# Optimization experiments

Measured on AMD Instinct MI355X. Metric: run time of the kernel, lower is better.

Reference implementation:

```python
import jax, jax.numpy as jnp
import numpy as np

NUM_HEADS = 12


def get_rel_pos(q_size, k_size, rel_pos):
    # rel_pos: (2*max(q,k)-1, C). Here q_size==k_size so no interpolation needed.
    q_coords = jnp.arange(q_size)[:, None] * max(k_size / q_size, 1.0)
    k_coords = jnp.arange(k_size)[None, :] * max(q_size / k_size, 1.0)
    rel = (q_coords - k_coords) + (k_size - 1) * max(q_size / k_size, 1.0)
    return rel_pos[rel.astype(jnp.int32)]  # (q_size, k_size, C)


def add_decomposed_rel_pos(attn, q, rel_pos_h, rel_pos_w, q_size, k_size):
    q_h, q_w = q_size
    k_h, k_w = k_size
    Rh = get_rel_pos(q_h, k_h, rel_pos_h)  # (q_h,k_h,C)
    Rw = get_rel_pos(q_w, k_w, rel_pos_w)  # (q_w,k_w,C)
    B, _, C = q.shape  # B = num_heads * batch
    r_q = q.reshape(B, q_h, q_w, C)
    rel_h = jnp.einsum('bhwc,hkc->bhwk', r_q, Rh)  # (B,q_h,q_w,k_h)
    rel_w = jnp.einsum('bhwc,wkc->bhwk', r_q, Rw)  # (B,q_h,q_w,k_w)
    attn = attn.reshape(B, q_h, q_w, k_h, k_w)
    attn = attn + rel_h[:, :, :, :, None] + rel_w[:, :, :, None, :]
    return attn.reshape(B, q_h * q_w, k_h * k_w)


def setup_inputs() -> dict:
    key = jax.random.key(0)
    ks = jax.random.split(key, 7)
    B, H, W, dim = 128, 14, 14, 768
    head_dim = dim // NUM_HEADS
    return {
        'x': jax.random.normal(ks[0], (B, H, W, dim), dtype=jnp.float32),
        'qkv_w': jax.random.normal(ks[1], (dim, 3 * dim), dtype=jnp.float32) * 0.02,
        'qkv_b': jax.random.normal(ks[2], (3 * dim,), dtype=jnp.float32) * 0.02,
        'proj_w': jax.random.normal(ks[3], (dim, dim), dtype=jnp.float32) * 0.02,
        'proj_b': jax.random.normal(ks[4], (dim,), dtype=jnp.float32) * 0.02,
        'rel_pos_h': jax.random.normal(ks[5], (2 * H - 1, head_dim), dtype=jnp.float32) * 0.02,
        'rel_pos_w': jax.random.normal(ks[6], (2 * W - 1, head_dim), dtype=jnp.float32) * 0.02,
    }


def reference(x, qkv_w, qkv_b, proj_w, proj_b, rel_pos_h, rel_pos_w):
    B, H, W, dim = x.shape
    nh = NUM_HEADS
    hd = dim // nh
    scale = hd ** -0.5
    L = H * W
    # qkv projection: (B,H,W,3*dim) -> (3, nh*B, L, hd)
    qkv = x.reshape(B, L, dim) @ qkv_w + qkv_b
    qkv = qkv.reshape(B, L, 3, nh, hd)
    qkv = jnp.transpose(qkv, (2, 3, 0, 1, 4)).reshape(3, nh * B, L, hd)
    q, k, v = qkv[0], qkv[1], qkv[2]
    attn = jnp.einsum('bqc,bkc->bqk', q * scale, k)  # (nh*B, L, L)
    attn = add_decomposed_rel_pos(attn, q, rel_pos_h, rel_pos_w, (H, W), (H, W))
    attn = jax.nn.softmax(attn, axis=-1)
    out = jnp.einsum('bqk,bkc->bqc', attn, v)  # (nh*B, L, hd)
    out = out.reshape(nh, B, H, W, hd)
    out = jnp.transpose(out, (1, 2, 3, 0, 4)).reshape(B, H, W, dim)
    return out @ proj_w + proj_b
```

## Files before the change

kernel.cpp:

```cpp
#include <hip/hip_runtime.h>
#include <stdint.h>

typedef unsigned short u16;
typedef __bf16 bf16x8 __attribute__((ext_vector_type(8)));
typedef u16 u16x8 __attribute__((ext_vector_type(8)));
typedef float f32x4 __attribute__((ext_vector_type(4)));

#define MFMA16(a,b,c) __builtin_amdgcn_mfma_f32_16x16x32_bf16((a),(b),(c),0,0,0)
#define GLOAD16(gp, lp) __builtin_amdgcn_global_load_lds( \
    (const __attribute__((address_space(1))) void*)(gp), \
    (__attribute__((address_space(3))) void*)(lp), 16, 0, 0)

__device__ __forceinline__ u16 f2bf(float f) {
  union { float f; uint32_t u; } v; v.f = f;
  return (u16)((v.u + 0x7FFFu + ((v.u >> 16) & 1u)) >> 16);
}
__device__ __forceinline__ float bits2f(uint32_t u) {
  union { uint32_t u; float f; } v; v.u = u; return v.f;
}
__device__ __forceinline__ uint32_t cvtpk(float lo, float hi) {
  uint32_t r;
  asm("v_cvt_pk_bf16_f32 %0, %1, %2" : "=v"(r) : "v"(lo), "v"(hi));
  return r;
}
__device__ __forceinline__ int4 pack8(const u16* v) {
  int4 r;
  r.x = (int)((uint32_t)v[0] | ((uint32_t)v[1] << 16));
  r.y = (int)((uint32_t)v[2] | ((uint32_t)v[3] << 16));
  r.z = (int)((uint32_t)v[4] | ((uint32_t)v[5] << 16));
  r.w = (int)((uint32_t)v[6] | ((uint32_t)v[7] << 16));
  return r;
}

__global__ void k_cvt(const float* __restrict__ in, u16* __restrict__ out, int n4) {
  int i = blockIdx.x * 256 + threadIdx.x;
  int stride = gridDim.x * 256;
  for (; i < n4; i += stride) {
    float4 v = reinterpret_cast<const float4*>(in)[i];
    ushort4 o;
    o.x = f2bf(v.x); o.y = f2bf(v.y); o.z = f2bf(v.z); o.w = f2bf(v.w);
    reinterpret_cast<ushort4*>(out)[i] = o;
  }
}

__global__ void k_transpose(const float* __restrict__ in, u16* __restrict__ out, int R, int C) {
  __shared__ float t[32][33];
  int tx = threadIdx.x & 31, ty = threadIdx.x >> 5;
  int c0 = blockIdx.x * 32, r0 = blockIdx.y * 32;
  #pragma unroll
  for (int i = 0; i < 4; i++)
    t[ty + i*8][tx] = in[(size_t)(r0 + ty + i*8) * C + (c0 + tx)];
  __syncthreads();
  #pragma unroll
  for (int i = 0; i < 4; i++)
    out[(size_t)(c0 + ty + i*8) * R + (r0 + tx)] = f2bf(t[tx][ty + i*8]);
}

__global__ __launch_bounds__(512, 2) void k_qkv256(
    const u16* __restrict__ A, const u16* __restrict__ BT, const float* __restrict__ bias,
    u16* __restrict__ qo, u16* __restrict__ ko, u16* __restrict__ vo)
{
  __shared__ u16 SMEM[65536];

  int bid0 = blockIdx.x;
  int xcd = bid0 & 7, idx = bid0 >> 3;
  int base = (xcd < 2) ? xcd * 111 : 2 * 111 + (xcd - 2) * 110;
  int wgid = base + idx;
  int mt = wgid / 9, nt = wgid - (wgid / 9) * 9;

  int tid = threadIdx.x, lane = tid & 63, w = tid >> 6;
  int g = lane >> 4, c4 = lane & 15;
  int wr = w >> 2, wc = w & 3;

  int srow = lane >> 2;
  int pslot = (lane & 3) ^ ((lane >> 3) & 3);
  int cidA = w * 2;

  const u16* pA1 = A + (size_t)(mt * 256 + cidA * 16 + srow) * 768 + pslot * 8;
  const u16* pA2 = pA1 + 16 * 768;
  const u16* pB1 = BT + (size_t)(nt * 256 + cidA * 16 + srow) * 768 + pslot * 8;
  const u16* pB2 = pB1 + 16 * 768;

  int rsel = g ^ ((c4 >> 1) & 3);
  int aoff = wr * 4096 + c4 * 32 + rsel * 8;
  int boff = wc * 2048 + c4 * 32 + rsel * 8;

  f32x4 acc[8][4];
  f32x4 z4 = {0.f, 0.f, 0.f, 0.f};
  #pragma unroll
  for (int f = 0; f < 8; f++)
    #pragma unroll
    for (int fc = 0; fc < 4; fc++) acc[f][fc] = z4;

  #pragma unroll
  for (int kk = 0; kk < 3; kk++) {
    u16* dA = SMEM + kk * 8192;
    GLOAD16(pA1 + kk * 32, dA + cidA * 512);
    GLOAD16(pA2 + kk * 32, dA + (cidA + 1) * 512);
    u16* dB = SMEM + 32768 + kk * 8192;
    GLOAD16(pB1 + kk * 32, dB + cidA * 512);
    GLOAD16(pB2 + kk * 32, dB + (cidA + 1) * 512);
  }
  asm volatile("s_waitcnt vmcnt(8)" ::: "memory");
  __builtin_amdgcn_s_barrier();

  for (int k = 0; k < 24; ++k) {
    const u16* As = SMEM + (k & 3) * 8192;
    const u16* Bs = SMEM + 32768 + (k & 3) * 8192;
    bf16x8 bfr[4], afr[4];
    #pragma unroll
    for (int fc = 0; fc < 4; fc++) bfr[fc] = *(const bf16x8*)(Bs + boff + fc * 512);
    #pragma unroll
    for (int f = 0; f < 4; f++) afr[f] = *(const bf16x8*)(As + aoff + f * 512);
    if (k < 21) {
      u16* d = SMEM + ((k + 3) & 3) * 8192;
      GLOAD16(pA1 + (k + 3) * 32, d + cidA * 512);
      GLOAD16(pA2 + (k + 3) * 32, d + (cidA + 1) * 512);
      asm volatile("s_waitcnt vmcnt(6)" ::: "memory");
    } else if (k == 21) {
      asm volatile("s_waitcnt vmcnt(0)" ::: "memory");
    }
    __builtin_amdgcn_s_barrier();
    __builtin_amdgcn_s_setprio(1);
    #pragma unroll
    for (int f = 0; f < 4; f++)
      #pragma unroll
      for (int fc = 0; fc < 4; fc++)
        acc[f][fc] = MFMA16(afr[f], bfr[fc], acc[f][fc]);
    __builtin_amdgcn_s_setprio(0);

    #pragma unroll
    for (int f = 0; f < 4; f++) afr[f] = *(const bf16x8*)(As + aoff + (4 + f) * 512);
    if (k < 21) {
      u16* d = SMEM + 32768 + ((k + 3) & 3) * 8192;
      GLOAD16(pB1 + (k + 3) * 32, d + cidA * 512);
      GLOAD16(pB2 + (k + 3) * 32, d + (cidA + 1) * 512);
      asm volatile("s_waitcnt vmcnt(6)" ::: "memory");
    }
    __builtin_amdgcn_s_barrier();
    __builtin_amdgcn_s_setprio(1);
    #pragma unroll
    for (int f = 0; f < 4; f++)
      #pragma unroll
      for (int fc = 0; fc < 4; fc++)
        acc[4 + f][fc] = MFMA16(afr[f], bfr[fc], acc[4 + f][fc]);
    __builtin_amdgcn_s_setprio(0);
  }

  int i3 = nt / 3;
  u16* dst = (i3 == 0) ? qo : (i3 == 1) ? ko : vo;
  int head = (nt - i3 * 3) * 4 + wc;
  float bsv[4];
  #pragma unroll
  for (int fc = 0; fc < 4; fc++) bsv[fc] = bias[nt * 256 + wc * 64 + fc * 16 + c4];

  int mbase = mt * 256 + wr * 128 + g * 4;
  #pragma unroll
  for (int f = 0; f < 8; f++) {
    #pragma unroll
    for (int j = 0; j < 4; j++) {
      int mm = mbase + f * 16 + j;
      int bb2 = mm / 196, ll = mm - bb2 * 196;
      size_t ro = (size_t)((head * 128 + bb2) * 196 + ll) * 64;
      #pragma unroll
      for (int fc = 0; fc < 4; fc++)
        dst[ro + fc * 16 + c4] = f2bf(acc[f][fc][j] + bsv[fc]);
    }
  }
}

__global__ __launch_bounds__(256, 2) void k_proj256(
    const u16* __restrict__ A, const u16* __restrict__ BT, const float* __restrict__ bias,
    float* __restrict__ out)
{
  __shared__ u16 SMEM[32768];

  int bid0 = blockIdx.x;
  int bid = (bid0 & 7) * 147 + (bid0 >> 3);
  int nt = bid % 6, mt = bid / 6;

  int tid = threadIdx.x, lane = tid & 63, w = tid >> 6;
  int g = lane >> 4, c4 = lane & 15;
  int wr = w >> 1, wc = w & 1;

  int srow = lane >> 2;
  int pslot = (lane & 3) ^ ((lane >> 3) & 3);
  int cidA = w * 2;

  const u16* pA1 = A + (size_t)(mt * 128 + cidA * 16 + srow) * 768 + pslot * 8;
  const u16* pA2 = pA1 + 16 * 768;
  const u16* pB1 = BT + (size_t)(nt * 128 + cidA * 16 + srow) * 768 + pslot * 8;
  const u16* pB2 = pB1 + 16 * 768;

  int rsel = g ^ ((c4 >> 1) & 3);
  int aoff = wr * 2048 + c4 * 32 + rsel * 8;
  int boff = wc * 2048 + c4 * 32 + rsel * 8;

  f32x4 acc[4][4];
  f32x4 z4 = {0.f, 0.f, 0.f, 0.f};
  #pragma unroll
  for (int f = 0; f < 4; f++)
    #pragma unroll
    for (int fc = 0; fc < 4; fc++) acc[f][fc] = z4;

  #pragma unroll
  for (int kk = 0; kk < 3; kk++) {
    u16* dA = SMEM + kk * 4096;
    GLOAD16(pA1 + kk * 32, dA + cidA * 512);
    GLOAD16(pA2 + kk * 32, dA + (cidA + 1) * 512);
    u16* dB = SMEM + 16384 + kk * 4096;
    GLOAD16(pB1 + kk * 32, dB + cidA * 512);
    GLOAD16(pB2 + kk * 32, dB + (cidA + 1) * 512);
  }
  asm volatile("s_waitcnt vmcnt(8)" ::: "memory");
  __builtin_amdgcn_s_barrier();

  for (int k = 0; k < 24; ++k) {
    const u16* As = SMEM + (k & 3) * 4096;
    const u16* Bs = SMEM + 16384 + (k & 3) * 4096;
    bf16x8 bfr[4], afr[4];
    #pragma unroll
    for (int fc = 0; fc < 4; fc++) bfr[fc] = *(const bf16x8*)(Bs + boff + fc * 512);
    #pragma unroll
    for (int f = 0; f < 4; f++) afr[f] = *(const bf16x8*)(As + aoff + f * 512);
    if (k < 21) {
      u16* dA = SMEM + ((k + 3) & 3) * 4096;
      GLOAD16(pA1 + (k + 3) * 32, dA + cidA * 512);
      GLOAD16(pA2 + (k + 3) * 32, dA + (cidA + 1) * 512);
      u16* dB = SMEM + 16384 + ((k + 3) & 3) * 4096;
      GLOAD16(pB1 + (k + 3) * 32, dB + cidA * 512);
      GLOAD16(pB2 + (k + 3) * 32, dB + (cidA + 1) * 512);
      asm volatile("s_waitcnt vmcnt(8)" ::: "memory");
    } else if (k == 21) {
      asm volatile("s_waitcnt vmcnt(4)" ::: "memory");
    } else if (k == 22) {
      asm volatile("s_waitcnt vmcnt(0)" ::: "memory");
    }
    __builtin_amdgcn_s_barrier();
    __builtin_amdgcn_s_setprio(1);
    #pragma unroll
    for (int f = 0; f < 4; f++)
      #pragma unroll
      for (int fc = 0; fc < 4; fc++)
        acc[f][fc] = MFMA16(afr[f], bfr[fc], acc[f][fc]);
    __builtin_amdgcn_s_setprio(0);
    __builtin_amdgcn_s_barrier();
  }

  #pragma unroll
  for (int fc = 0; fc < 4; fc++) {
    int n0 = nt * 128 + wc * 64 + fc * 16 + c4;
    float bs = bias[n0];
    #pragma unroll
    for (int fr = 0; fr < 4; fr++)
      #pragma unroll
      for (int j = 0; j < 4; j++) {
        int m = mt * 128 + wr * 64 + fr * 16 + g * 4 + j;
        out[(size_t)m * 768 + n0] = acc[fr][fc][j] + bs;
      }
  }
}

#define VP 232
__global__ __launch_bounds__(256, 2) void k_attn(
    const u16* __restrict__ Q, const u16* __restrict__ Kg, const u16* __restrict__ Vg,
    const u16* __restrict__ RPH, const u16* __restrict__ RPW, u16* __restrict__ Ows)
{
  __shared__ u16 K64[208 * 64];
  __shared__ u16 Krel[208 * 40];
  __shared__ u16 VT[64 * VP];
  __shared__ u16 Qrel[4][16 * 40];

  int bh = blockIdx.x;
  int hh = bh >> 7, bb = bh & 127;
  int tid = threadIdx.x, lane = tid & 63, w = tid >> 6;
  int g = lane >> 4, c4 = lane & 15;

  const u16* kbase = Kg + (size_t)bh * 12544;
  const u16* vbase = Vg + (size_t)bh * 12544;
  const u16* qbase = Q + (size_t)bh * 12544;

  for (int ch = tid; ch < 1664; ch += 256) {
    int row = ch >> 3, s = ch & 7;
    u16 outv[8];
    if (row < 196) {
      u16x8 v = *(const u16x8*)(kbase + row * 64 + s * 8);
      #pragma unroll
      for (int e = 0; e < 8; e++)
        outv[e] = f2bf(bits2f((uint32_t)v[e] << 16) * 0.125f);
    } else {
      #pragma unroll
      for (int e = 0; e < 8; e++) outv[e] = 0;
    }
    *(int4*)(K64 + row * 64 + ((s ^ (row & 7)) * 8)) = pack8(outv);
  }
  if (tid < 208) {
    int k = tid;
    int kh = k / 14, kw2 = k - kh * 14;
    #pragma unroll
    for (int s = 0; s < 5; s++) {
      u16 vals[8];
      #pragma unroll
      for (int e = 0; e < 8; e++) {
        int c = s * 8 + e;
        u16 x = 0;
        if (k < 196) {
          if (c == kh) x = 0x3F80;
          else if (c == 14 + kw2) x = 0x3F80;
        } else {
          if (c == 28) x = 0x3F80;
        }
        vals[e] = x;
      }
      *(int4*)(Krel + k * 40 + s * 8) = pack8(vals);
    }
  }
  for (int i = tid; i < 2048; i += 256) {
    int chn = i >> 5, c = 192 + (i & 31);
    if (c >= 196 && c < VP) VT[chn * VP + c] = 0;
  }
  for (int ch2 = tid; ch2 < 784; ch2 += 256) {
    int kp = ch2 >> 3, cb = ch2 & 7;
    int key = kp * 2, cz = cb * 8;
    u16x8 a = *(const u16x8*)(vbase + key * 64 + cz);
    u16x8 b2 = *(const u16x8*)(vbase + (key + 1) * 64 + cz);
    int kk = key & 31;
    int colp = (key >> 5) * 32 + ((kk & 15) >> 2) * 8 + (kk & 3) + ((kk >> 4) << 2);
    #pragma unroll
    for (int j = 0; j < 8; j++) {
      uint32_t pk = (uint32_t)a[j] | ((uint32_t)b2[j] << 16);
      *(uint32_t*)(VT + (cz + j) * VP + colp) = pk;
    }
  }
  __syncthreads();

  int t1 = 16 + c4; if (t1 > 26) t1 = 26;
  bf16x8 rh00 = *(const bf16x8*)(RPH + c4 * 64 + g * 8);
  bf16x8 rh01 = *(const bf16x8*)(RPH + c4 * 64 + 32 + g * 8);
  bf16x8 rh10 = *(const bf16x8*)(RPH + t1 * 64 + g * 8);
  bf16x8 rh11 = *(const bf16x8*)(RPH + t1 * 64 + 32 + g * 8);
  bf16x8 rw00 = *(const bf16x8*)(RPW + c4 * 64 + g * 8);
  bf16x8 rw01 = *(const bf16x8*)(RPW + c4 * 64 + 32 + g * 8);
  bf16x8 rw10 = *(const bf16x8*)(RPW + t1 * 64 + g * 8);
  bf16x8 rw11 = *(const bf16x8*)(RPW + t1 * 64 + 32 + g * 8);

  f32x4 z4 = {0.f, 0.f, 0.f, 0.f};

  for (int qt = w; qt < 13; qt += 4) {
    int qi = qt * 16 + c4;
    int qrow = qi > 195 ? 195 : qi;
    bf16x8 qa0 = *(const bf16x8*)(qbase + qrow * 64 + g * 8);
    bf16x8 qa1 = *(const bf16x8*)(qbase + qrow * 64 + 32 + g * 8);

    u16* Qr = (u16*)Qrel[w];
    {
      int4 zz = {0, 0, 0, 0};
      *(int4*)(Qr + lane * 8) = zz;
      if (lane < 16) *(int4*)(Qr + 512 + lane * 8) = zz;
      if (g == 0) Qr[c4 * 40 + 28] = f2bf(-30000.f);
    }

    int qh = qi / 14;
    int qwv = qi - qh * 14;

    f32x4 e0 = MFMA16(rh00, qa0, z4); e0 = MFMA16(rh01, qa1, e0);
    f32x4 e1 = MFMA16(rh10, qa0, z4); e1 = MFMA16(rh11, qa1, e1);
    #pragma unroll
    for (int tt = 0; tt < 2; tt++) {
      f32x4 e = tt ? e1 : e0;
      #pragma unroll
      for (int j = 0; j < 4; j++) {
        int t = tt * 16 + 4 * g + j;
        int kh = qh + 13 - t;
        if ((unsigned)kh <= 13u) Qr[c4 * 40 + kh] = f2bf(e[j]);
      }
    }
    f32x4 f0 = MFMA16(rw00, qa0, z4); f0 = MFMA16(rw01, qa1, f0);
    f32x4 f1 = MFMA16(rw10, qa0, z4); f1 = MFMA16(rw11, qa1, f1);
    #pragma unroll
    for (int tt = 0; tt < 2; tt++) {
      f32x4 e = tt ? f1 : f0;
      #pragma unroll
      for (int j = 0; j < 4; j++) {
        int t = tt * 16 + 4 * g + j;
        int kw3 = qwv + 13 - t;
        if ((unsigned)kw3 <= 13u) Qr[c4 * 40 + 14 + kw3] = f2bf(e[j]);
      }
    }

    bf16x8 qrelB = *(const bf16x8*)(Qr + c4 * 40 + g * 8);

    f32x4 St[13];
    #pragma unroll
    for (int i = 0; i < 13; i++) {
      int key = i * 16 + c4;
      const u16* kr = K64 + key * 64;
      int sw = key & 7;
      bf16x8 kb0 = *(const bf16x8*)(kr + ((g ^ sw) * 8));
      bf16x8 kb1 = *(const bf16x8*)(kr + (((4 + g) ^ sw) * 8));
      f32x4 acc = MFMA16(kb0, qa0, z4);
      acc = MFMA16(kb1, qa1, acc);
      bf16x8 krl = *(const bf16x8*)(Krel + key * 40 + g * 8);
      St[i] = MFMA16(krl, qrelB, acc);
    }

    float mx = -3.0e38f;
    #pragma unroll
    for (int i = 0; i < 13; i++)
      #pragma unroll
      for (int j = 0; j < 4; j++) mx = fmaxf(mx, St[i][j]);
    mx = fmaxf(mx, __shfl_xor(mx, 16));
    mx = fmaxf(mx, __shfl_xor(mx, 32));

    float ls = 0.f;
    f32x4 O[4] = {z4, z4, z4, z4};
    #pragma unroll
    for (int p = 0; p < 7; p++) {
      float pe[8];
      #pragma unroll
      for (int j2 = 0; j2 < 4; j2++) { pe[j2] = __expf(St[2 * p][j2] - mx); ls += pe[j2]; }
      if (p < 6) {
        #pragma unroll
        for (int j2 = 0; j2 < 4; j2++) { pe[4 + j2] = __expf(St[2 * p + 1][j2] - mx); ls += pe[4 + j2]; }
      } else {
        #pragma unroll
        for (int j2 = 0; j2 < 4; j2++) pe[4 + j2] = 0.f;
      }
      union { uint32_t u[4]; bf16x8 v; } pb;
      pb.u[0] = cvtpk(pe[0], pe[1]);
      pb.u[1] = cvtpk(pe[2], pe[3]);
      pb.u[2] = cvtpk(pe[4], pe[5]);
      pb.u[3] = cvtpk(pe[6], pe[7]);
      #pragma unroll
      for (int ct = 0; ct < 4; ct++) {
        bf16x8 va = *(const bf16x8*)(VT + (ct * 16 + c4) * VP + p * 32 + g * 8);
        O[ct] = MFMA16(va, pb.v, O[ct]);
      }
    }
    ls += __shfl_xor(ls, 16);
    ls += __shfl_xor(ls, 32);

    if (qi < 196) {
      float inv = 1.f / ls;
      size_t obase = (size_t)(bb * 196 + qi) * 768 + hh * 64;
      #pragma unroll
      for (int ct = 0; ct < 4; ct++) {
        uint32_t o0 = cvtpk(O[ct][0] * inv, O[ct][1] * inv);
        uint32_t o1 = cvtpk(O[ct][2] * inv, O[ct][3] * inv);
        uint2 ov = {o0, o1};
        *(uint2*)(Ows + obase + ct * 16 + g * 4) = ov;
      }
    }
  }
}

extern "C" void kernel_launch(void* const* d_in, const int* in_sizes, int n_in,
                              void* d_out, int out_size, void* d_ws, size_t ws_size,
                              hipStream_t stream) {
  (void)in_sizes; (void)n_in; (void)out_size; (void)ws_size;
  const float* x      = (const float*)d_in[0];
  const float* qkv_w  = (const float*)d_in[1];
  const float* qkv_b  = (const float*)d_in[2];
  const float* proj_w = (const float*)d_in[3];
  const float* proj_b = (const float*)d_in[4];
  const float* rph    = (const float*)d_in[5];
  const float* rpw    = (const float*)d_in[6];
  float* out = (float*)d_out;
  char* ws = (char*)d_ws;

  u16* xb   = (u16*)(ws);
  u16* wT   = (u16*)(ws + 38535168);
  u16* pT   = (u16*)(ws + 42074112);
  u16* rphb = (u16*)(ws + 43253760);
  u16* rpwb = (u16*)(ws + 43257856);
  u16* qws  = (u16*)(ws + 43261952);
  u16* kws  = (u16*)(ws + 81797120);
  u16* vws  = (u16*)(ws + 120332288);
  u16* Ows  = xb;

  k_cvt<<<2048, 256, 0, stream>>>(x, xb, 4816896);
  k_cvt<<<2, 256, 0, stream>>>(rph, rphb, 432);
  k_cvt<<<2, 256, 0, stream>>>(rpw, rpwb, 432);
  k_transpose<<<dim3(72, 24), 256, 0, stream>>>(qkv_w, wT, 768, 2304);
  k_transpose<<<dim3(24, 24), 256, 0, stream>>>(proj_w, pT, 768, 768);
  k_qkv256<<<882, 512, 0, stream>>>(xb, wT, qkv_b, qws, kws, vws);
  k_attn<<<1536, 256, 0, stream>>>(qws, kws, vws, rphb, rpwb, Ows);
  k_proj256<<<1176, 256, 0, stream>>>(Ows, pT, proj_b, out);
}
```

Baseline: 263.8 us.

## Fold log2e into K and rel-pos scaling, use exp2, prefetch Q, reorder V transpose

Folds the log2(e) factor into the K scale (0.125*log2e) and into the bf16 rel-pos tables, so the softmax can use exp2f instead of __expf with no per-element multiply. Q fragments for the next query tile are prefetched one iteration ahead. The V transpose loop is reindexed so consecutive threads take consecutive key pairs, which changes the LDS write pattern. The proj fragment reads move into a helper with no behaviour change. Rounding the scaled values to bf16 shifts numerics slightly, and the -30000 mask sentinel is not rescaled.

Measured after the change: 272.0 us. 3.1% more time.

```diff
diff --git a/kernel.cpp b/kernel.cpp
--- a/kernel.cpp
+++ b/kernel.cpp
@@ -1,5 +1,6 @@
 #include <hip/hip_runtime.h>
 #include <stdint.h>
+#include <math.h>
 
 typedef unsigned short u16;
 typedef __bf16 bf16x8 __attribute__((ext_vector_type(8)));
@@ -32,13 +33,14 @@
   return r;
 }
 
-__global__ void k_cvt(const float* __restrict__ in, u16* __restrict__ out, int n4) {
+__global__ void k_cvt(const float* __restrict__ in, u16* __restrict__ out, int n4, float scale) {
   int i = blockIdx.x * 256 + threadIdx.x;
   int stride = gridDim.x * 256;
   for (; i < n4; i += stride) {
     float4 v = reinterpret_cast<const float4*>(in)[i];
     ushort4 o;
-    o.x = f2bf(v.x); o.y = f2bf(v.y); o.z = f2bf(v.z); o.w = f2bf(v.w);
+    o.x = f2bf(v.x * scale); o.y = f2bf(v.y * scale);
+    o.z = f2bf(v.z * scale); o.w = f2bf(v.w * scale);
     reinterpret_cast<ushort4*>(out)[i] = o;
   }
 }
@@ -169,6 +171,14 @@
   }
 }
 
+__device__ __forceinline__ void rd_frags8(const u16* As_, const u16* Bs_, int aoff, int boff,
+                                          bf16x8 (&b)[4], bf16x8 (&a)[4]) {
+  #pragma unroll
+  for (int fc = 0; fc < 4; fc++) b[fc] = *(const bf16x8*)(Bs_ + boff + fc * 512);
+  #pragma unroll
+  for (int f = 0; f < 4; f++) a[f] = *(const bf16x8*)(As_ + aoff + f * 512);
+}
+
 __global__ __launch_bounds__(256, 2) void k_proj256(
     const u16* __restrict__ A, const u16* __restrict__ BT, const float* __restrict__ bias,
     float* __restrict__ out)
@@ -219,10 +229,7 @@
     const u16* As = SMEM + (k & 3) * 4096;
     const u16* Bs = SMEM + 16384 + (k & 3) * 4096;
     bf16x8 bfr[4], afr[4];
-    #pragma unroll
-    for (int fc = 0; fc < 4; fc++) bfr[fc] = *(const bf16x8*)(Bs + boff + fc * 512);
-    #pragma unroll
-    for (int f = 0; f < 4; f++) afr[f] = *(const bf16x8*)(As + aoff + f * 512);
+    rd_frags8(As, Bs, aoff, boff, bfr, afr);
     if (k < 21) {
       u16* dA = SMEM + ((k + 3) & 3) * 4096;
       GLOAD16(pA1 + (k + 3) * 32, dA + cidA * 512);
@@ -280,6 +287,7 @@
   const u16* vbase = Vg + (size_t)bh * 12544;
   const u16* qbase = Q + (size_t)bh * 12544;
 
+  const float KSC = 0.18033688011f;
   for (int ch = tid; ch < 1664; ch += 256) {
     int row = ch >> 3, s = ch & 7;
     u16 outv[8];
@@ -287,7 +295,7 @@
       u16x8 v = *(const u16x8*)(kbase + row * 64 + s * 8);
       #pragma unroll
       for (int e = 0; e < 8; e++)
-        outv[e] = f2bf(bits2f((uint32_t)v[e] << 16) * 0.125f);
+        outv[e] = f2bf(bits2f((uint32_t)v[e] << 16) * KSC);
     } else {
       #pragma unroll
       for (int e = 0; e < 8; e++) outv[e] = 0;
@@ -320,7 +328,7 @@
     if (c >= 196 && c < VP) VT[chn * VP + c] = 0;
   }
   for (int ch2 = tid; ch2 < 784; ch2 += 256) {
-    int kp = ch2 >> 3, cb = ch2 & 7;
+    int kp = ch2 % 98, cb = ch2 / 98;
     int key = kp * 2, cz = cb * 8;
     u16x8 a = *(const u16x8*)(vbase + key * 64 + cz);
     u16x8 b2 = *(const u16x8*)(vbase + (key + 1) * 64 + cz);
@@ -346,11 +354,20 @@
 
   f32x4 z4 = {0.f, 0.f, 0.f, 0.f};
 
+  int qi0 = w * 16 + c4;
+  int qr0 = qi0 > 195 ? 195 : qi0;
+  bf16x8 qa0 = *(const bf16x8*)(qbase + qr0 * 64 + g * 8);
+  bf16x8 qa1 = *(const bf16x8*)(qbase + qr0 * 64 + 32 + g * 8);
+
   for (int qt = w; qt < 13; qt += 4) {
     int qi = qt * 16 + c4;
-    int qrow = qi > 195 ? 195 : qi;
-    bf16x8 qa0 = *(const bf16x8*)(qbase + qrow * 64 + g * 8);
-    bf16x8 qa1 = *(const bf16x8*)(qbase + qrow * 64 + 32 + g * 8);
+    bf16x8 nq0, nq1;
+    int qn = qt + 4;
+    if (qn < 13) {
+      int qrn = qn * 16 + c4; if (qrn > 195) qrn = 195;
+      nq0 = *(const bf16x8*)(qbase + qrn * 64 + g * 8);
+      nq1 = *(const bf16x8*)(qbase + qrn * 64 + 32 + g * 8);
+    }
 
     u16* Qr = (u16*)Qrel[w];
     {
@@ -418,10 +435,10 @@
     for (int p = 0; p < 7; p++) {
       float pe[8];
       #pragma unroll
-      for (int j2 = 0; j2 < 4; j2++) { pe[j2] = __expf(St[2 * p][j2] - mx); ls += pe[j2]; }
+      for (int j2 = 0; j2 < 4; j2++) { pe[j2] = exp2f(St[2 * p][j2] - mx); ls += pe[j2]; }
       if (p < 6) {
         #pragma unroll
-        for (int j2 = 0; j2 < 4; j2++) { pe[4 + j2] = __expf(St[2 * p + 1][j2] - mx); ls += pe[4 + j2]; }
+        for (int j2 = 0; j2 < 4; j2++) { pe[4 + j2] = exp2f(St[2 * p + 1][j2] - mx); ls += pe[4 + j2]; }
       } else {
         #pragma unroll
         for (int j2 = 0; j2 < 4; j2++) pe[4 + j2] = 0.f;
@@ -451,6 +468,7 @@
         *(uint2*)(Ows + obase + ct * 16 + g * 4) = ov;
       }
     }
+    qa0 = nq0; qa1 = nq1;
   }
 }
 
@@ -478,9 +496,10 @@
   u16* vws  = (u16*)(ws + 120332288);
   u16* Ows  = xb;
 
-  k_cvt<<<2048, 256, 0, stream>>>(x, xb, 4816896);
-  k_cvt<<<2, 256, 0, stream>>>(rph, rphb, 432);
-  k_cvt<<<2, 256, 0, stream>>>(rpw, rpwb, 432);
+  const float LOG2E = 1.44269504f;
+  k_cvt<<<2048, 256, 0, stream>>>(x, xb, 4816896, 1.0f);
+  k_cvt<<<2, 256, 0, stream>>>(rph, rphb, 432, LOG2E);
+  k_cvt<<<2, 256, 0, stream>>>(rpw, rpwb, 432, LOG2E);
   k_transpose<<<dim3(72, 24), 256, 0, stream>>>(qkv_w, wT, 768, 2304);
   k_transpose<<<dim3(24, 24), 256, 0, stream>>>(proj_w, pT, 768, 768);
   k_qkv256<<<882, 512, 0, stream>>>(xb, wT, qkv_b, qws, kws, vws);
```
